# Kernel tuning notes

Hardware: AMD Instinct MI355X
Metric: run time of the kernel (lower is better)

The kernel has to match this reference:

```python
import jax, jax.numpy as jnp
import numpy as np

DIM = 1024
HEADS = 16
DIM_HEAD = 64
INNER = HEADS * DIM_HEAD  # 1024
MLP = 4096
EPS = 1e-5


def layer_norm(x, gamma, beta):
    mu = jnp.mean(x, axis=-1, keepdims=True)
    var = jnp.var(x, axis=-1, keepdims=True)
    return (x - mu) * jax.lax.rsqrt(var + EPS) * gamma + beta


def setup_inputs() -> dict:
    key = jax.random.key(0)
    ks = jax.random.split(key, 10)
    s = 0.02
    return {
        "x": jax.random.normal(ks[0], (2, 2048, DIM), dtype=jnp.float32),
        "ln1_g": jnp.ones((DIM,), jnp.float32),
        "ln1_b": jnp.zeros((DIM,), jnp.float32),
        "w_qkv": jax.random.normal(ks[1], (DIM, 3 * INNER), jnp.float32) * s,
        "w_out": jax.random.normal(ks[2], (INNER, DIM), jnp.float32) * s,
        "b_out": jnp.zeros((DIM,), jnp.float32),
        "ln2_g": jnp.ones((DIM,), jnp.float32),
        "ln2_b": jnp.zeros((DIM,), jnp.float32),
        "w1": jax.random.normal(ks[3], (DIM, MLP), jnp.float32) * s,
        "b1": jnp.zeros((MLP,), jnp.float32),
        "w2": jax.random.normal(ks[4], (MLP, DIM), jnp.float32) * s,
        "b2": jnp.zeros((DIM,), jnp.float32),
    }


def reference(x, ln1_g, ln1_b, w_qkv, w_out, b_out, ln2_g, ln2_b, w1, b1, w2, b2):
    b, n, _ = x.shape
    scale = DIM_HEAD ** -0.5

    # --- attention sublayer (pre-norm) ---
    h = layer_norm(x, ln1_g, ln1_b)
    qkv = h @ w_qkv  # [b, n, 3*inner]
    q, k, v = jnp.split(qkv, 3, axis=-1)
    # [b, n, inner] -> [b, heads, n, dim_head]
    def to_heads(t):
        return t.reshape(b, n, HEADS, DIM_HEAD).transpose(0, 2, 1, 3)
    q, k, v = to_heads(q), to_heads(k), to_heads(v)
    dots = jnp.einsum('bhid,bhjd->bhij', q, k) * scale  # [b,h,n,n]
    attn = jax.nn.softmax(dots, axis=-1)
    out = jnp.einsum('bhij,bhjd->bhid', attn, v)
    out = out.transpose(0, 2, 1, 3).reshape(b, n, INNER)
    x = out @ w_out + b_out + x

    # --- FFN sublayer (pre-norm) ---
    h = layer_norm(x, ln2_g, ln2_b)
    h = jax.nn.gelu(h @ w1 + b1, approximate=False)
    x = h @ w2 + b2 + x
    return x
```

## Files before the change

### kernel.cpp

```cpp
#include <hip/hip_runtime.h>
#include <hip/hip_bf16.h>
#include <math.h>

#define SEQ 2048
#define BATCH 2
#define TOKENS 4096
#define HEADS 16
#define DHEAD 64
#define TOKSTRIDE 3072

typedef __attribute__((ext_vector_type(4))) float f32x4;
typedef __attribute__((ext_vector_type(16))) float f32x16;
typedef __attribute__((ext_vector_type(8))) __bf16 bf16x8;
typedef __attribute__((ext_vector_type(8))) unsigned short ushort8;
typedef __attribute__((ext_vector_type(4))) unsigned short ushort4_t;
typedef __attribute__((ext_vector_type(4))) unsigned u32x4;
typedef __attribute__((ext_vector_type(2))) unsigned u32x2;

#if __has_builtin(__builtin_amdgcn_exp2f)
#define EXP2(x) __builtin_amdgcn_exp2f(x)
#else
#define EXP2(x) exp2f(x)
#endif

#if __has_builtin(__builtin_amdgcn_permlane32_swap)
#define HAS_PL32 1
#else
#define HAS_PL32 0
#endif

__device__ __forceinline__ unsigned short f2bf(float f) {
  unsigned u = __builtin_bit_cast(unsigned, f);
  u += 0x7fffu + ((u >> 16) & 1u);
  return (unsigned short)(u >> 16);
}

__device__ __forceinline__ float bf2f(unsigned short s) {
  unsigned u = ((unsigned)s) << 16;
  return __builtin_bit_cast(float, u);
}

__device__ __forceinline__ unsigned cvt_pk_bf16(float lo, float hi) {
  unsigned r;
  asm("v_cvt_pk_bf16_f32 %0, %1, %2" : "=v"(r) : "v"(lo), "v"(hi));
  return r;
}

__device__ __forceinline__ void cp16(const void* g, void* l) {
  __builtin_amdgcn_global_load_lds((const __attribute__((address_space(1))) void*)g,
                                   (__attribute__((address_space(3))) void*)l, 16, 0, 0);
}

__global__ __launch_bounds__(256) void ln_rows(const float* __restrict__ x,
                                               const float* __restrict__ g,
                                               const float* __restrict__ b,
                                               unsigned short* __restrict__ out) {
  const int row = blockIdx.x;
  const int t = threadIdx.x;
  const f32x4* x4 = (const f32x4*)(x + (size_t)row * 1024);
  f32x4 v = x4[t];
  float sum = v[0] + v[1] + v[2] + v[3];
  float ss  = v[0]*v[0] + v[1]*v[1] + v[2]*v[2] + v[3]*v[3];
#pragma unroll
  for (int off = 1; off < 64; off <<= 1) {
    sum += __shfl_xor(sum, off);
    ss  += __shfl_xor(ss, off);
  }
  __shared__ float red[8];
  const int w = t >> 6, l = t & 63;
  if (l == 0) { red[w] = sum; red[w + 4] = ss; }
  __syncthreads();
  sum = red[0] + red[1] + red[2] + red[3];
  ss  = red[4] + red[5] + red[6] + red[7];
  const float mean = sum * (1.0f / 1024.0f);
  const float var  = ss * (1.0f / 1024.0f) - mean * mean;
  const float rs = rsqrtf(var + 1e-5f);
  ushort4_t o;
#pragma unroll
  for (int j = 0; j < 4; ++j) {
    float gv = g[t * 4 + j], bv = b[t * 4 + j];
    o[j] = f2bf((v[j] - mean) * rs * gv + bv);
  }
  *(ushort4_t*)(out + (size_t)row * 1024 + t * 4) = o;
}

__global__ __launch_bounds__(256) void ln_rows_bf(const unsigned short* __restrict__ x,
                                                  const float* __restrict__ g,
                                                  const float* __restrict__ b,
                                                  unsigned short* __restrict__ out) {
  const int row = blockIdx.x;
  const int t = threadIdx.x;
  ushort4_t v4 = *(const ushort4_t*)(x + (size_t)row * 1024 + t * 4);
  float v[4] = {bf2f(v4[0]), bf2f(v4[1]), bf2f(v4[2]), bf2f(v4[3])};
  float sum = v[0] + v[1] + v[2] + v[3];
  float ss  = v[0]*v[0] + v[1]*v[1] + v[2]*v[2] + v[3]*v[3];
#pragma unroll
  for (int off = 1; off < 64; off <<= 1) {
    sum += __shfl_xor(sum, off);
    ss  += __shfl_xor(ss, off);
  }
  __shared__ float red[8];
  const int w = t >> 6, l = t & 63;
  if (l == 0) { red[w] = sum; red[w + 4] = ss; }
  __syncthreads();
  sum = red[0] + red[1] + red[2] + red[3];
  ss  = red[4] + red[5] + red[6] + red[7];
  const float mean = sum * (1.0f / 1024.0f);
  const float var  = ss * (1.0f / 1024.0f) - mean * mean;
  const float rs = rsqrtf(var + 1e-5f);
  ushort4_t o;
#pragma unroll
  for (int j = 0; j < 4; ++j) {
    float gv = g[t * 4 + j], bv = b[t * 4 + j];
    o[j] = f2bf((v[j] - mean) * rs * gv + bv);
  }
  *(ushort4_t*)(out + (size_t)row * 1024 + t * 4) = o;
}

__global__ __launch_bounds__(256) void transpose_cast(const float* __restrict__ w,
                                                      unsigned short* __restrict__ wt,
                                                      int K, int N, float scale, int nscaled) {
  __shared__ float tile[32][33];
  const int n0 = blockIdx.x * 32, k0 = blockIdx.y * 32;
  const int tx = threadIdx.x & 31;
  const int ty = threadIdx.x >> 5;
#pragma unroll
  for (int i = 0; i < 4; ++i)
    tile[ty + 8 * i][tx] = w[(size_t)(k0 + ty + 8 * i) * N + n0 + tx];
  __syncthreads();
#pragma unroll
  for (int i = 0; i < 4; ++i) {
    int n = n0 + ty + 8 * i;
    float s = (n < nscaled) ? scale : 1.0f;
    wt[(size_t)n * K + k0 + tx] = f2bf(tile[tx][ty + 8 * i] * s);
  }
}

template <int EPI, int BN, int MINW>
__global__ __launch_bounds__(256, MINW) void gemm_bt(
    const unsigned short* __restrict__ A, const unsigned short* __restrict__ Bt,
    void* __restrict__ Cp, const float* __restrict__ bias, const void* __restrict__ resv,
    int M, int N, int K) {
  constexpr int BM = 128, BK = 64;
  constexpr int MR = BM / 32, NR = BN / 32;
  constexpr int AIT = BM * BK / 2048;
  constexpr int BIT = BN * BK / 2048;
  __shared__ unsigned short la[BM * BK];
  __shared__ unsigned short lb[BN * BK];
  const int t = threadIdx.x;
  const int w = t >> 6, l = t & 63;
  const int nwg = gridDim.x;
  const int bid = blockIdx.x;
  const int bid2 = (bid & 7) * (nwg >> 3) + (bid >> 3);
  const int nx = N / BN;
  const int m0 = (bid2 / nx) * BM, n0 = (bid2 % nx) * BN;
  const int wr = w >> 1, wc = w & 1;
  const int lrow = l & 15, lk4 = l >> 4;
  f32x4 acc[MR][NR] = {};

  for (int k0 = 0; k0 < K; k0 += BK) {
#pragma unroll
    for (int i = 0; i < AIT; ++i) {
      int idx = t + 256 * i;
      int row = idx >> 3, seg = idx & 7;
      int ss = seg ^ (row & 7);
      cp16(A + (size_t)(m0 + row) * K + k0 + ss * 8, (char*)la + w * 1024 + i * 4096);
    }
#pragma unroll
    for (int i = 0; i < BIT; ++i) {
      int idx = t + 256 * i;
      int row = idx >> 3, seg = idx & 7;
      int ss = seg ^ (row & 7);
      cp16(Bt + (size_t)(n0 + row) * K + k0 + ss * 8, (char*)lb + w * 1024 + i * 4096);
    }
    __syncthreads();
#pragma unroll
    for (int ks = 0; ks < 2; ++ks) {
      bf16x8 af[MR], bfr[NR];
#pragma unroll
      for (int mi = 0; mi < MR; ++mi) {
        int row = wr * (BM / 2) + mi * 16 + lrow;
        int ss = (ks * 4 + lk4) ^ (row & 7);
        af[mi] = *(const bf16x8*)((const char*)la + row * 128 + ss * 16);
      }
#pragma unroll
      for (int ni = 0; ni < NR; ++ni) {
        int row = wc * (BN / 2) + ni * 16 + lrow;
        int ss = (ks * 4 + lk4) ^ (row & 7);
        bfr[ni] = *(const bf16x8*)((const char*)lb + row * 128 + ss * 16);
      }
#pragma unroll
      for (int mi = 0; mi < MR; ++mi)
#pragma unroll
        for (int ni = 0; ni < NR; ++ni)
          acc[mi][ni] = __builtin_amdgcn_mfma_f32_16x16x32_bf16(af[mi], bfr[ni], acc[mi][ni], 0, 0, 0);
    }
    __syncthreads();
  }

#pragma unroll
  for (int mi = 0; mi < MR; ++mi) {
    int rowb = m0 + wr * (BM / 2) + mi * 16 + lk4 * 4;
#pragma unroll
    for (int ni = 0; ni < NR; ++ni) {
      int col = n0 + wc * (BN / 2) + ni * 16 + lrow;
      f32x4 a = acc[mi][ni];
#pragma unroll
      for (int r = 0; r < 4; ++r) {
        size_t off = (size_t)(rowb + r) * N + col;
        if (EPI == 0) {
          ((unsigned short*)Cp)[off] = f2bf(a[r]);
        } else if (EPI == 2) {
          float v = a[r] + bias[col];
          ((unsigned short*)Cp)[off] = f2bf(0.5f * v * (1.0f + erff(v * 0.70710678f)));
        } else if (EPI == 3) {
          ((unsigned short*)Cp)[off] = f2bf(a[r] + bias[col] + ((const float*)resv)[off]);
        } else {
          ((float*)Cp)[off] = a[r] + bias[col] + bf2f(((const unsigned short*)resv)[off]);
        }
      }
    }
  }
}

__global__ __launch_bounds__(256, 2) void attn2(const unsigned short* __restrict__ qkv,
                                                unsigned short* __restrict__ Op,
                                                float2* __restrict__ ml) {
  __shared__ unsigned short lk_[2][64 * 64];
  __shared__ unsigned short lvt[2][64 * 64];
  const int t = threadIdx.x, wv = t >> 6, l = t & 63;
  const int chunk = blockIdx.x & 1, qb = blockIdx.x >> 1;
  const int h = blockIdx.y, b = blockIdx.z;
  const size_t tok0 = (size_t)b * SEQ;
  const int lq = l & 31, hi = l >> 5, l7 = l & 7;
  const int qrow = qb * 128 + wv * 32 + lq;
  const int kstart = chunk * 16;

  bf16x8 qf[4];
#pragma unroll
  for (int dc = 0; dc < 4; ++dc)
    qf[dc] = *(const bf16x8*)(qkv + (tok0 + qrow) * TOKSTRIDE + h * DHEAD + dc * 16 + hi * 8);

  float mrun = -1e30f, lsum = 0.0f;
  f32x16 o0 = {}, o1 = {};

  {
#pragma unroll
    for (int i = 0; i < 2; ++i) {
      int idx = t + 256 * i;
      int key = idx >> 3, seg = idx & 7;
      cp16(qkv + (tok0 + kstart * 64 + key) * TOKSTRIDE + 1024 + h * DHEAD + ((seg ^ (key & 7)) << 3),
           (char*)lk_[0] + wv * 1024 + i * 4096);
    }
#pragma unroll
    for (int i = 0; i < 2; ++i) {
      int idx = t + 256 * i;
      int key = idx & 63, seg = idx >> 6;
      ushort8 v8 = *(const ushort8*)(qkv + (tok0 + kstart * 64 + key) * TOKSTRIDE + 2048 + h * DHEAD + seg * 8);
#pragma unroll
      for (int j = 0; j < 8; ++j) {
        int d = seg * 8 + j;
        lvt[0][d * 64 + (((key >> 3) ^ (d & 7)) << 3) + (key & 7)] = v8[j];
      }
    }
  }
  __syncthreads();

  int cur = 0;
  for (int kb = 0; kb < 16; ++kb) {
    const int nxt = cur ^ 1;
    const int kpre = kstart + ((kb + 1 < 16) ? kb + 1 : kb);
#pragma unroll
    for (int i = 0; i < 2; ++i) {
      int idx = t + 256 * i;
      int key = idx >> 3, seg = idx & 7;
      cp16(qkv + (tok0 + kpre * 64 + key) * TOKSTRIDE + 1024 + h * DHEAD + ((seg ^ (key & 7)) << 3),
           (char*)lk_[nxt] + wv * 1024 + i * 4096);
    }
    ushort8 vpre[2];
#pragma unroll
    for (int i = 0; i < 2; ++i) {
      int idx = t + 256 * i;
      int key = idx & 63, seg = idx >> 6;
      vpre[i] = *(const ushort8*)(qkv + (tok0 + kpre * 64 + key) * TOKSTRIDE + 2048 + h * DHEAD + seg * 8);
    }

    f32x16 s0 = {}, s1 = {};
    __builtin_amdgcn_s_setprio(1);
#pragma unroll
    for (int dc = 0; dc < 4; ++dc) {
      int sgA = (dc * 2 + hi) ^ l7;
      bf16x8 kf0 = *(const bf16x8*)((const char*)lk_[cur] + lq * 128 + (sgA << 4));
      bf16x8 kf1 = *(const bf16x8*)((const char*)lk_[cur] + (32 + lq) * 128 + (sgA << 4));
      s0 = __builtin_amdgcn_mfma_f32_32x32x16_bf16(kf0, qf[dc], s0, 0, 0, 0);
      s1 = __builtin_amdgcn_mfma_f32_32x32x16_bf16(kf1, qf[dc], s1, 0, 0, 0);
    }
    __builtin_amdgcn_s_setprio(0);

    float mx[8];
#pragma unroll
    for (int r = 0; r < 8; ++r)
      mx[r] = fmaxf(fmaxf(s0[r], s0[r + 8]), fmaxf(s1[r], s1[r + 8]));
#pragma unroll
    for (int r = 0; r < 4; ++r) mx[r] = fmaxf(mx[r], mx[r + 4]);
    float m01 = fmaxf(fmaxf(mx[0], mx[1]), fmaxf(mx[2], mx[3]));
    float pm = fmaxf(m01, __shfl_xor(m01, 32));

    if (__any(pm > mrun + 8.0f)) {
      float mn = fmaxf(mrun, pm);
      float alpha = EXP2(mrun - mn);
      mrun = mn;
      lsum *= alpha;
#pragma unroll
      for (int r = 0; r < 16; ++r) {
        int qi = (r & 3) + 8 * (r >> 2) + 4 * hi;
        float ar = __shfl(alpha, qi);
        o0[r] *= ar; o1[r] *= ar;
      }
    }

    float p0[16], p1[16], ts[16];
#pragma unroll
    for (int r = 0; r < 16; ++r) { p0[r] = EXP2(s0[r] - mrun); }
#pragma unroll
    for (int r = 0; r < 16; ++r) { p1[r] = EXP2(s1[r] - mrun); }
#pragma unroll
    for (int r = 0; r < 16; ++r) ts[r] = p0[r] + p1[r];
#pragma unroll
    for (int st = 8; st > 0; st >>= 1)
#pragma unroll
      for (int r = 0; r < 8; ++r)
        if (r < st) ts[r] += ts[r + st];
    float psum = ts[0] + __shfl_xor(ts[0], 32);
    lsum += psum;

    unsigned W0[8], W1[8];
#pragma unroll
    for (int mI = 0; mI < 8; ++mI) {
      W0[mI] = cvt_pk_bf16(p0[2 * mI], p0[2 * mI + 1]);
      W1[mI] = cvt_pk_bf16(p1[2 * mI], p1[2 * mI + 1]);
    }
#if !HAS_PL32
    unsigned X0[8], X1[8];
#pragma unroll
    for (int mI = 0; mI < 8; ++mI) {
      X0[mI] = __shfl_xor((int)W0[mI], 32);
      X1[mI] = __shfl_xor((int)W1[mI], 32);
    }
#endif

    __builtin_amdgcn_s_setprio(1);
#pragma unroll
    for (int kt = 0; kt < 2; ++kt) {
#pragma unroll
      for (int c = 0; c < 2; ++c) {
        u32x4 fw;
#if HAS_PL32
        unsigned a0 = (kt == 0) ? W0[4 * c + 0] : W1[4 * c + 0];
        unsigned a1 = (kt == 0) ? W0[4 * c + 1] : W1[4 * c + 1];
        unsigned b0 = (kt == 0) ? W0[4 * c + 2] : W1[4 * c + 2];
        unsigned b1 = (kt == 0) ? W0[4 * c + 3] : W1[4 * c + 3];
        u32x2 pa = __builtin_amdgcn_permlane32_swap(a0, b0, false, false);
        u32x2 pb = __builtin_amdgcn_permlane32_swap(a1, b1, false, false);
        fw[0] = pa[0]; fw[1] = pb[0]; fw[2] = pa[1]; fw[3] = pb[1];
#else
        if (kt == 0) {
          fw[0] = hi ? X0[4 * c + 2] : W0[4 * c + 0];
          fw[1] = hi ? X0[4 * c + 3] : W0[4 * c + 1];
          fw[2] = hi ? W0[4 * c + 2] : X0[4 * c + 0];
          fw[3] = hi ? W0[4 * c + 3] : X0[4 * c + 1];
        } else {
          fw[0] = hi ? X1[4 * c + 2] : W1[4 * c + 0];
          fw[1] = hi ? X1[4 * c + 3] : W1[4 * c + 1];
          fw[2] = hi ? W1[4 * c + 2] : X1[4 * c + 0];
          fw[3] = hi ? W1[4 * c + 3] : X1[4 * c + 1];
        }
#endif
        bf16x8 pf = __builtin_bit_cast(bf16x8, fw);
        int ksg = (kt * 4 + c * 2 + hi) ^ l7;
        bf16x8 vfA = *(const bf16x8*)((const char*)lvt[cur] + lq * 128 + (ksg << 4));
        bf16x8 vfB = *(const bf16x8*)((const char*)lvt[cur] + (32 + lq) * 128 + (ksg << 4));
        o0 = __builtin_amdgcn_mfma_f32_32x32x16_bf16(pf, vfA, o0, 0, 0, 0);
        o1 = __builtin_amdgcn_mfma_f32_32x32x16_bf16(pf, vfB, o1, 0, 0, 0);
      }
    }
    __builtin_amdgcn_s_setprio(0);

#pragma unroll
    for (int i = 0; i < 2; ++i) {
      int idx = t + 256 * i;
      int key = idx & 63, seg = idx >> 6;
#pragma unroll
      for (int j = 0; j < 8; ++j) {
        int d = seg * 8 + j;
        lvt[nxt][d * 64 + (((key >> 3) ^ (d & 7)) << 3) + (key & 7)] = vpre[i][j];
      }
    }
    __syncthreads();
    cur = nxt;
  }

  const size_t cbase = (size_t)chunk * TOKENS;
#pragma unroll
  for (int r = 0; r < 16; ++r) {
    int qi = (r & 3) + 8 * (r >> 2) + 4 * hi;
    size_t rowoff = (cbase + tok0 + qb * 128 + wv * 32 + qi) * (size_t)1024 + h * DHEAD;
    Op[rowoff + lq]      = f2bf(o0[r]);
    Op[rowoff + 32 + lq] = f2bf(o1[r]);
  }
  if (l < 32) {
    size_t tokr = tok0 + qb * 128 + wv * 32 + lq;
    ml[(cbase + tokr) * 16 + h] = make_float2(mrun, lsum);
  }
}

__global__ __launch_bounds__(256) void attn_combine(const unsigned short* __restrict__ Op,
                                                    const float2* __restrict__ ml,
                                                    unsigned short* __restrict__ out) {
  const int t = threadIdx.x, w = t >> 6, l = t & 63;
  const size_t tok = blockIdx.x * 4 + w;
#pragma unroll
  for (int h = 0; h < 16; ++h) {
    float2 a = ml[tok * 16 + h];
    float2 c = ml[((size_t)TOKENS + tok) * 16 + h];
    float M = fmaxf(a.x, c.x);
    float w0 = EXP2(a.x - M), w1 = EXP2(c.x - M);
    float inv = 1.0f / (a.y * w0 + c.y * w1);
    int col = h * 64 + l;
    float o = (bf2f(Op[tok * 1024 + col]) * w0 +
               bf2f(Op[((size_t)TOKENS + tok) * 1024 + col]) * w1) * inv;
    out[tok * 1024 + col] = f2bf(o);
  }
}

extern "C" void kernel_launch(void* const* d_in, const int* in_sizes, int n_in,
                              void* d_out, int out_size, void* d_ws, size_t ws_size,
                              hipStream_t stream) {
  const float* x    = (const float*)d_in[0];
  const float* ln1g = (const float*)d_in[1];
  const float* ln1b = (const float*)d_in[2];
  const float* wqkv = (const float*)d_in[3];
  const float* wout = (const float*)d_in[4];
  const float* bout = (const float*)d_in[5];
  const float* ln2g = (const float*)d_in[6];
  const float* ln2b = (const float*)d_in[7];
  const float* w1   = (const float*)d_in[8];
  const float* b1   = (const float*)d_in[9];
  const float* w2   = (const float*)d_in[10];
  const float* b2   = (const float*)d_in[11];

  char* ws = (char*)d_ws;
  unsigned short* wqkvT = (unsigned short*)ws; ws += (size_t)3072 * 1024 * 2;
  unsigned short* woutT = (unsigned short*)ws; ws += (size_t)1024 * 1024 * 2;
  unsigned short* w1T   = (unsigned short*)ws; ws += (size_t)4096 * 1024 * 2;
  unsigned short* w2T   = (unsigned short*)ws; ws += (size_t)1024 * 4096 * 2;
  unsigned short* h1    = (unsigned short*)ws; ws += (size_t)TOKENS * 1024 * 2;
  unsigned short* qkvb  = (unsigned short*)ws; ws += (size_t)TOKENS * 3072 * 2;
  unsigned short* attno = (unsigned short*)ws; ws += (size_t)TOKENS * 1024 * 2;
  unsigned short* xa    = (unsigned short*)ws; ws += (size_t)TOKENS * 1024 * 4;
  unsigned short* h2    = (unsigned short*)ws; ws += (size_t)TOKENS * 1024 * 2;
  unsigned short* hid   = (unsigned short*)ws; ws += (size_t)TOKENS * 4096 * 2;
  float2*         mlbuf = (float2*)ws;         ws += (size_t)2 * TOKENS * 16 * 8;
  unsigned short* Opart = hid;

  transpose_cast<<<dim3(3072 / 32, 1024 / 32), 256, 0, stream>>>(wqkv, wqkvT, 1024, 3072, 0.18033688f, 1024);
  transpose_cast<<<dim3(1024 / 32, 1024 / 32), 256, 0, stream>>>(wout, woutT, 1024, 1024, 1.0f, 0);
  transpose_cast<<<dim3(4096 / 32, 1024 / 32), 256, 0, stream>>>(w1, w1T, 1024, 4096, 1.0f, 0);
  transpose_cast<<<dim3(1024 / 32, 4096 / 32), 256, 0, stream>>>(w2, w2T, 4096, 1024, 1.0f, 0);

  ln_rows<<<TOKENS, 256, 0, stream>>>(x, ln1g, ln1b, h1);
  gemm_bt<0, 128, 2><<<768, 256, 0, stream>>>(h1, wqkvT, qkvb, nullptr, nullptr, TOKENS, 3072, 1024);
  attn2<<<dim3(2 * SEQ / 128, HEADS, BATCH), 256, 0, stream>>>(qkvb, Opart, mlbuf);
  attn_combine<<<TOKENS / 4, 256, 0, stream>>>(Opart, mlbuf, attno);
  gemm_bt<3, 64, 3><<<512, 256, 0, stream>>>(attno, woutT, xa, bout, x, TOKENS, 1024, 1024);
  ln_rows_bf<<<TOKENS, 256, 0, stream>>>(xa, ln2g, ln2b, h2);
  gemm_bt<2, 128, 2><<<1024, 256, 0, stream>>>(h2, w1T, hid, b1, nullptr, TOKENS, 4096, 1024);
  gemm_bt<4, 64, 3><<<512, 256, 0, stream>>>(hid, w2T, (float*)d_out, b2, xa, TOKENS, 1024, 4096);
}
```

Before: 253.7 us.

## Add 256x256 8-wave ping-pong GEMM kernel for the FFN up-projection

```diff
diff --git a/kernel.cpp b/kernel.cpp
--- a/kernel.cpp
+++ b/kernel.cpp
@@ -50,6 +50,9 @@
   __builtin_amdgcn_global_load_lds((const __attribute__((address_space(1))) void*)g,
                                    (__attribute__((address_space(3))) void*)l, 16, 0, 0);
 }
+
+#define FENCE asm volatile("" ::: "memory")
+#define BARR  do { FENCE; __builtin_amdgcn_s_barrier(); FENCE; } while (0)
 
 __global__ __launch_bounds__(256) void ln_rows(const float* __restrict__ x,
                                                const float* __restrict__ g,
@@ -217,6 +220,122 @@
           ((unsigned short*)Cp)[off] = f2bf(a[r] + bias[col] + ((const float*)resv)[off]);
         } else {
           ((float*)Cp)[off] = a[r] + bias[col] + bf2f(((const unsigned short*)resv)[off]);
+        }
+      }
+    }
+  }
+}
+
+template <int EPI>
+__global__ __launch_bounds__(512, 2) void gemm8p(
+    const unsigned short* __restrict__ A, const unsigned short* __restrict__ Bt,
+    void* __restrict__ Cp, const float* __restrict__ bias, int M, int N, int K) {
+  __shared__ char lds[131072];
+  const int t = threadIdx.x, w = t >> 6, l = t & 63;
+  const int lrow = l & 15, lk4 = l >> 4;
+  const int wr = w >> 2, wc = w & 3;
+  const int nwg = gridDim.x, bid = blockIdx.x;
+  const int bid2 = (bid & 7) * (nwg >> 3) + (bid >> 3);
+  const int nx = N / 256;
+  const int m0 = (bid2 / nx) * 256, n0 = (bid2 % nx) * 256;
+  const int NT = K >> 6;
+  const int segsrc = (l & 7) ^ ((l >> 3) & 7);
+  f32x4 acc[8][4] = {};
+
+#define STGA(kt, half)                                                              \
+  {                                                                                 \
+    _Pragma("unroll") for (int u = 0; u < 2; ++u) {                                 \
+      int rl = w * 8 + (l >> 3) + 64 * u;                                           \
+      int row = (half) * 64 + (rl & 63) + (rl >> 6) * 128;                          \
+      cp16(A + (size_t)(m0 + row) * K + (kt) * 64 + segsrc * 8,                     \
+           lds + ((kt) & 1) * 65536 + (half) * 8192 + u * 16384 + w * 1024);        \
+    }                                                                               \
+  }
+#define STGB(kt, half)                                                              \
+  {                                                                                 \
+    _Pragma("unroll") for (int u = 0; u < 2; ++u) {                                 \
+      int rl = w * 8 + (l >> 3) + 64 * u;                                           \
+      int row = (rl >> 5) * 64 + (half) * 32 + (rl & 31);                           \
+      cp16(Bt + (size_t)(n0 + row) * K + (kt) * 64 + segsrc * 8,                    \
+           lds + ((kt) & 1) * 65536 + 32768 +                                       \
+               (((w >> 2) + 2 * u) * 64 + (half) * 32 + (w & 3) * 8) * 128);        \
+    }                                                                               \
+  }
+#define RDA(kt, mh, AF)                                                             \
+  _Pragma("unroll") for (int mi = 0; mi < 4; ++mi)                                  \
+  _Pragma("unroll") for (int ks = 0; ks < 2; ++ks) {                                \
+    int row = wr * 128 + (mh) * 64 + mi * 16 + lrow;                                \
+    AF[mi][ks] = *(const bf16x8*)(lds + ((kt) & 1) * 65536 + row * 128 +            \
+                                  (((ks * 4 + lk4) ^ (row & 7)) << 4));             \
+  }
+#define RDB(kt, nh, BF)                                                             \
+  _Pragma("unroll") for (int ni = 0; ni < 2; ++ni)                                  \
+  _Pragma("unroll") for (int ks = 0; ks < 2; ++ks) {                                \
+    int row = wc * 64 + (nh) * 32 + ni * 16 + lrow;                                 \
+    BF[ni][ks] = *(const bf16x8*)(lds + ((kt) & 1) * 65536 + 32768 + row * 128 +    \
+                                  (((ks * 4 + lk4) ^ (row & 7)) << 4));             \
+  }
+#define MF(mh, nh, AF, BF)                                                          \
+  __builtin_amdgcn_s_setprio(1);                                                    \
+  _Pragma("unroll") for (int mi = 0; mi < 4; ++mi)                                  \
+  _Pragma("unroll") for (int ni = 0; ni < 2; ++ni)                                  \
+  _Pragma("unroll") for (int ks = 0; ks < 2; ++ks)                                  \
+    acc[(mh) * 4 + mi][(nh) * 2 + ni] = __builtin_amdgcn_mfma_f32_16x16x32_bf16(    \
+        AF[mi][ks], BF[ni][ks], acc[(mh) * 4 + mi][(nh) * 2 + ni], 0, 0, 0);        \
+  __builtin_amdgcn_s_setprio(0);
+
+  STGA(0, 0); STGB(0, 0); STGB(0, 1); STGA(0, 1);
+  STGA(1, 0); STGB(1, 0); STGB(1, 1);
+  asm volatile("s_waitcnt vmcnt(6)" ::: "memory");
+  BARR;
+
+  bf16x8 af[4][2], bfL[2][2], bfH[2][2];
+  for (int T = 0; T < NT; ++T) {
+    RDA(T, 0, af); RDB(T, 0, bfL);
+    if (T + 1 < NT) STGA(T + 1, 1);
+    BARR;
+    MF(0, 0, af, bfL);
+    BARR;
+    RDB(T, 1, bfH);
+    if (T + 2 < NT) STGA(T + 2, 0);
+    BARR;
+    MF(0, 1, af, bfH);
+    BARR;
+    RDA(T, 1, af);
+    if (T + 2 < NT) STGB(T + 2, 0);
+    BARR;
+    MF(1, 1, af, bfH);
+    BARR;
+    if (T + 2 < NT) STGB(T + 2, 1);
+    BARR;
+    MF(1, 0, af, bfL);
+    if (T + 1 < NT) {
+      if (T + 1 <= NT - 2) { asm volatile("s_waitcnt vmcnt(6)" ::: "memory"); }
+      else                 { asm volatile("s_waitcnt vmcnt(0)" ::: "memory"); }
+    }
+    BARR;
+  }
+#undef STGA
+#undef STGB
+#undef RDA
+#undef RDB
+#undef MF
+
+#pragma unroll
+  for (int mi8 = 0; mi8 < 8; ++mi8) {
+    int rowb = m0 + wr * 128 + mi8 * 16 + lk4 * 4;
+#pragma unroll
+    for (int ni4 = 0; ni4 < 4; ++ni4) {
+      int col = n0 + wc * 64 + ni4 * 16 + lrow;
+      f32x4 a = acc[mi8][ni4];
+#pragma unroll
+      for (int r = 0; r < 4; ++r) {
+        size_t off = (size_t)(rowb + r) * N + col;
+        if (EPI == 0) {
+          ((unsigned short*)Cp)[off] = f2bf(a[r]);
+        } else {
+          float v = a[r] + bias[col];
+          ((unsigned short*)Cp)[off] = f2bf(0.5f * v * (1.0f + erff(v * 0.70710678f)));
         }
       }
     }
@@ -474,6 +593,6 @@
   attn_combine<<<TOKENS / 4, 256, 0, stream>>>(Opart, mlbuf, attno);
   gemm_bt<3, 64, 3><<<512, 256, 0, stream>>>(attno, woutT, xa, bout, x, TOKENS, 1024, 1024);
   ln_rows_bf<<<TOKENS, 256, 0, stream>>>(xa, ln2g, ln2b, h2);
-  gemm_bt<2, 128, 2><<<1024, 256, 0, stream>>>(h2, w1T, hid, b1, nullptr, TOKENS, 4096, 1024);
+  gemm8p<2><<<256, 512, 0, stream>>>(h2, w1T, hid, b1, TOKENS, 4096, 1024);
   gemm_bt<4, 64, 3><<<512, 256, 0, stream>>>(hid, w2T, (float*)d_out, b2, xa, TOKENS, 1024, 4096);
 }
```

After: 255.2 us. Within noise of the previous version (+0.6%).

## Split attention keys into four chunks and single-buffer K/V shared memory

Applied to the files above, without the earlier changes.

```diff
diff --git a/kernel.cpp b/kernel.cpp
--- a/kernel.cpp
+++ b/kernel.cpp
@@ -50,6 +50,9 @@
   __builtin_amdgcn_global_load_lds((const __attribute__((address_space(1))) void*)g,
                                    (__attribute__((address_space(3))) void*)l, 16, 0, 0);
 }
+
+#define FENCE asm volatile("" ::: "memory")
+#define BARR  do { FENCE; __builtin_amdgcn_s_barrier(); FENCE; } while (0)
 
 __global__ __launch_bounds__(256) void ln_rows(const float* __restrict__ x,
                                                const float* __restrict__ g,
@@ -223,18 +226,18 @@
   }
 }
 
-__global__ __launch_bounds__(256, 2) void attn2(const unsigned short* __restrict__ qkv,
+__global__ __launch_bounds__(256, 2) void attn4(const unsigned short* __restrict__ qkv,
                                                 unsigned short* __restrict__ Op,
                                                 float2* __restrict__ ml) {
-  __shared__ unsigned short lk_[2][64 * 64];
-  __shared__ unsigned short lvt[2][64 * 64];
+  __shared__ unsigned short lk_[64 * 64];
+  __shared__ unsigned short lvt[64 * 64];
   const int t = threadIdx.x, wv = t >> 6, l = t & 63;
-  const int chunk = blockIdx.x & 1, qb = blockIdx.x >> 1;
+  const int chunk = blockIdx.x & 3, qb = blockIdx.x >> 2;
   const int h = blockIdx.y, b = blockIdx.z;
   const size_t tok0 = (size_t)b * SEQ;
   const int lq = l & 31, hi = l >> 5, l7 = l & 7;
   const int qrow = qb * 128 + wv * 32 + lq;
-  const int kstart = chunk * 16;
+  const int kstart = chunk * 8;
 
   bf16x8 qf[4];
 #pragma unroll
@@ -250,7 +253,7 @@
       int idx = t + 256 * i;
       int key = idx >> 3, seg = idx & 7;
       cp16(qkv + (tok0 + kstart * 64 + key) * TOKSTRIDE + 1024 + h * DHEAD + ((seg ^ (key & 7)) << 3),
-           (char*)lk_[0] + wv * 1024 + i * 4096);
+           (char*)lk_ + wv * 1024 + i * 4096);
     }
 #pragma unroll
     for (int i = 0; i < 2; ++i) {
@@ -260,42 +263,48 @@
 #pragma unroll
       for (int j = 0; j < 8; ++j) {
         int d = seg * 8 + j;
-        lvt[0][d * 64 + (((key >> 3) ^ (d & 7)) << 3) + (key & 7)] = v8[j];
+        lvt[d * 64 + (((key >> 3) ^ (d & 7)) << 3) + (key & 7)] = v8[j];
       }
     }
   }
   __syncthreads();
 
-  int cur = 0;
-  for (int kb = 0; kb < 16; ++kb) {
-    const int nxt = cur ^ 1;
-    const int kpre = kstart + ((kb + 1 < 16) ? kb + 1 : kb);
-#pragma unroll
-    for (int i = 0; i < 2; ++i) {
-      int idx = t + 256 * i;
-      int key = idx >> 3, seg = idx & 7;
-      cp16(qkv + (tok0 + kpre * 64 + key) * TOKSTRIDE + 1024 + h * DHEAD + ((seg ^ (key & 7)) << 3),
-           (char*)lk_[nxt] + wv * 1024 + i * 4096);
-    }
-    ushort8 vpre[2];
-#pragma unroll
-    for (int i = 0; i < 2; ++i) {
-      int idx = t + 256 * i;
-      int key = idx & 63, seg = idx >> 6;
-      vpre[i] = *(const ushort8*)(qkv + (tok0 + kpre * 64 + key) * TOKSTRIDE + 2048 + h * DHEAD + seg * 8);
-    }
+  for (int kb = 0; kb < 8; ++kb) {
+    const bool more = (kb + 1 < 8);
+    const int kpre = kstart + kb + 1;
 
     f32x16 s0 = {}, s1 = {};
     __builtin_amdgcn_s_setprio(1);
 #pragma unroll
     for (int dc = 0; dc < 4; ++dc) {
       int sgA = (dc * 2 + hi) ^ l7;
-      bf16x8 kf0 = *(const bf16x8*)((const char*)lk_[cur] + lq * 128 + (sgA << 4));
-      bf16x8 kf1 = *(const bf16x8*)((const char*)lk_[cur] + (32 + lq) * 128 + (sgA << 4));
+      bf16x8 kf0 = *(const bf16x8*)((const char*)lk_ + lq * 128 + (sgA << 4));
+      bf16x8 kf1 = *(const bf16x8*)((const char*)lk_ + (32 + lq) * 128 + (sgA << 4));
       s0 = __builtin_amdgcn_mfma_f32_32x32x16_bf16(kf0, qf[dc], s0, 0, 0, 0);
       s1 = __builtin_amdgcn_mfma_f32_32x32x16_bf16(kf1, qf[dc], s1, 0, 0, 0);
     }
     __builtin_amdgcn_s_setprio(0);
+
+    asm volatile("s_waitcnt lgkmcnt(0)" ::: "memory");
+    BARR;
+    __builtin_amdgcn_sched_barrier(0);
+
+    ushort8 vpre[2];
+    if (more) {
+#pragma unroll
+      for (int i = 0; i < 2; ++i) {
+        int idx = t + 256 * i;
+        int key = idx >> 3, seg = idx & 7;
+        cp16(qkv + (tok0 + kpre * 64 + key) * TOKSTRIDE + 1024 + h * DHEAD + ((seg ^ (key & 7)) << 3),
+             (char*)lk_ + wv * 1024 + i * 4096);
+      }
+#pragma unroll
+      for (int i = 0; i < 2; ++i) {
+        int idx = t + 256 * i;
+        int key = idx & 63, seg = idx >> 6;
+        vpre[i] = *(const ushort8*)(qkv + (tok0 + kpre * 64 + key) * TOKSTRIDE + 2048 + h * DHEAD + seg * 8);
+      }
+    }
 
     float mx[8];
 #pragma unroll
@@ -378,26 +387,33 @@
 #endif
         bf16x8 pf = __builtin_bit_cast(bf16x8, fw);
         int ksg = (kt * 4 + c * 2 + hi) ^ l7;
-        bf16x8 vfA = *(const bf16x8*)((const char*)lvt[cur] + lq * 128 + (ksg << 4));
-        bf16x8 vfB = *(const bf16x8*)((const char*)lvt[cur] + (32 + lq) * 128 + (ksg << 4));
+        bf16x8 vfA = *(const bf16x8*)((const char*)lvt + lq * 128 + (ksg << 4));
+        bf16x8 vfB = *(const bf16x8*)((const char*)lvt + (32 + lq) * 128 + (ksg << 4));
         o0 = __builtin_amdgcn_mfma_f32_32x32x16_bf16(pf, vfA, o0, 0, 0, 0);
         o1 = __builtin_amdgcn_mfma_f32_32x32x16_bf16(pf, vfB, o1, 0, 0, 0);
       }
     }
     __builtin_amdgcn_s_setprio(0);
 
-#pragma unroll
-    for (int i = 0; i < 2; ++i) {
-      int idx = t + 256 * i;
-      int key = idx & 63, seg = idx >> 6;
-#pragma unroll
-      for (int j = 0; j < 8; ++j) {
-        int d = seg * 8 + j;
-        lvt[nxt][d * 64 + (((key >> 3) ^ (d & 7)) << 3) + (key & 7)] = vpre[i][j];
-      }
-    }
-    __syncthreads();
-    cur = nxt;
+    asm volatile("s_waitcnt lgkmcnt(0)" ::: "memory");
+    BARR;
+    __builtin_amdgcn_sched_barrier(0);
+
+    if (more) {
+#pragma unroll
+      for (int i = 0; i < 2; ++i) {
+        int idx = t + 256 * i;
+        int key = idx & 63, seg = idx >> 6;
+#pragma unroll
+        for (int j = 0; j < 8; ++j) {
+          int d = seg * 8 + j;
+          lvt[d * 64 + (((key >> 3) ^ (d & 7)) << 3) + (key & 7)] = vpre[i][j];
+        }
+      }
+    }
+    asm volatile("s_waitcnt vmcnt(0) lgkmcnt(0)" ::: "memory");
+    BARR;
+    __builtin_amdgcn_sched_barrier(0);
   }
 
   const size_t cbase = (size_t)chunk * TOKENS;
@@ -414,22 +430,28 @@
   }
 }
 
-__global__ __launch_bounds__(256) void attn_combine(const unsigned short* __restrict__ Op,
-                                                    const float2* __restrict__ ml,
-                                                    unsigned short* __restrict__ out) {
+__global__ __launch_bounds__(256) void attn_combine4(const unsigned short* __restrict__ Op,
+                                                     const float2* __restrict__ ml,
+                                                     unsigned short* __restrict__ out) {
   const int t = threadIdx.x, w = t >> 6, l = t & 63;
   const size_t tok = blockIdx.x * 4 + w;
 #pragma unroll
   for (int h = 0; h < 16; ++h) {
-    float2 a = ml[tok * 16 + h];
-    float2 c = ml[((size_t)TOKENS + tok) * 16 + h];
-    float M = fmaxf(a.x, c.x);
-    float w0 = EXP2(a.x - M), w1 = EXP2(c.x - M);
-    float inv = 1.0f / (a.y * w0 + c.y * w1);
+    float2 mm[4];
+#pragma unroll
+    for (int c = 0; c < 4; ++c) mm[c] = ml[((size_t)c * TOKENS + tok) * 16 + h];
+    float M = fmaxf(fmaxf(mm[0].x, mm[1].x), fmaxf(mm[2].x, mm[3].x));
+    float wgt[4];
+    float den = 0.0f;
+#pragma unroll
+    for (int c = 0; c < 4; ++c) { wgt[c] = EXP2(mm[c].x - M); den += mm[c].y * wgt[c]; }
+    float inv = 1.0f / den;
     int col = h * 64 + l;
-    float o = (bf2f(Op[tok * 1024 + col]) * w0 +
-               bf2f(Op[((size_t)TOKENS + tok) * 1024 + col]) * w1) * inv;
-    out[tok * 1024 + col] = f2bf(o);
+    float o = 0.0f;
+#pragma unroll
+    for (int c = 0; c < 4; ++c)
+      o += bf2f(Op[((size_t)c * TOKENS + tok) * 1024 + col]) * wgt[c];
+    out[tok * 1024 + col] = f2bf(o * inv);
   }
 }
 
@@ -460,7 +482,7 @@
   unsigned short* xa    = (unsigned short*)ws; ws += (size_t)TOKENS * 1024 * 4;
   unsigned short* h2    = (unsigned short*)ws; ws += (size_t)TOKENS * 1024 * 2;
   unsigned short* hid   = (unsigned short*)ws; ws += (size_t)TOKENS * 4096 * 2;
-  float2*         mlbuf = (float2*)ws;         ws += (size_t)2 * TOKENS * 16 * 8;
+  float2*         mlbuf = (float2*)ws;         ws += (size_t)4 * TOKENS * 16 * 8;
   unsigned short* Opart = hid;
 
   transpose_cast<<<dim3(3072 / 32, 1024 / 32), 256, 0, stream>>>(wqkv, wqkvT, 1024, 3072, 0.18033688f, 1024);
@@ -470,8 +492,8 @@
 
   ln_rows<<<TOKENS, 256, 0, stream>>>(x, ln1g, ln1b, h1);
   gemm_bt<0, 128, 2><<<768, 256, 0, stream>>>(h1, wqkvT, qkvb, nullptr, nullptr, TOKENS, 3072, 1024);
-  attn2<<<dim3(2 * SEQ / 128, HEADS, BATCH), 256, 0, stream>>>(qkvb, Opart, mlbuf);
-  attn_combine<<<TOKENS / 4, 256, 0, stream>>>(Opart, mlbuf, attno);
+  attn4<<<dim3(4 * SEQ / 128, HEADS, BATCH), 256, 0, stream>>>(qkvb, Opart, mlbuf);
+  attn_combine4<<<TOKENS / 4, 256, 0, stream>>>(Opart, mlbuf, attno);
   gemm_bt<3, 64, 3><<<512, 256, 0, stream>>>(attno, woutT, xa, bout, x, TOKENS, 1024, 1024);
   ln_rows_bf<<<TOKENS, 256, 0, stream>>>(xa, ln2g, ln2b, h2);
   gemm_bt<2, 128, 2><<<1024, 256, 0, stream>>>(h2, w1T, hid, b1, nullptr, TOKENS, 4096, 1024);
```

New measurement: 247.4 us. -2.5%, faster.
